# Kernel tuning notes

Hardware: AMD Instinct MI355X
Metric: run time of the kernel (lower is better)

## Reference

```python
import jax, jax.numpy as jnp
import numpy as np

B, T, D, H = 8, 2048, 1024, 128  # batch, seq (== block_size), n_embd, head_size


def setup_inputs() -> dict:
    key = jax.random.key(0)
    kx, kq, kk, kv = jax.random.split(key, 4)
    s = D ** -0.5  # rough linear-init scale
    return {
        "x": jax.random.normal(kx, (B, T, D), dtype=jnp.float32),
        "Wq": jax.random.normal(kq, (D, H), dtype=jnp.float32) * s,
        "Wk": jax.random.normal(kk, (D, H), dtype=jnp.float32) * s,
        "Wv": jax.random.normal(kv, (D, H), dtype=jnp.float32) * s,
    }


def reference(x, Wq, Wk, Wv):
    # Linear projections (no bias)
    q = x @ Wq  # [B, T, H]
    k = x @ Wk  # [B, T, H]
    v = x @ Wv  # [B, T, H]
    scale = k.shape[-1] ** -0.5
    scores = jnp.einsum("bth,bsh->bts", q, k) * scale  # [B, T, T]
    # causal mask from tril buffer
    causal = jnp.tril(jnp.ones((T, T), dtype=bool))
    scores = jnp.where(causal, scores, jnp.finfo(scores.dtype).min)
    att = jax.nn.softmax(scores, axis=-1)
    out = jnp.einsum("bts,bsh->bth", att, v)  # [B, T, H]
    return out
```

## Files before the change

### kernel.cpp

```cpp
#include <hip/hip_runtime.h>
#include <hip/hip_bf16.h>
#include <stdint.h>

typedef float f32x4 __attribute__((ext_vector_type(4)));
typedef __bf16 bf16x8 __attribute__((ext_vector_type(8)));

#define T_SEQ 2048
#define D_EMB 1024
#define H_DIM 128
#define NBATCH 8
#define NTOK 16384

typedef __attribute__((address_space(3))) uint32_t lds_u32;
typedef const __attribute__((address_space(1))) uint32_t glb_u32;

#define DPPF(x, ctrl)                                                    \
  __int_as_float(__builtin_amdgcn_update_dpp(                            \
      0, __float_as_int(x), (ctrl), 0xF, 0xF, true))


__global__ __launch_bounds__(256) void prep_w_kernel(
    const float* __restrict__ Wq, const float* __restrict__ Wk,
    const float* __restrict__ Wv, __hip_bfloat16* __restrict__ Wt) {
  const int mat = blockIdx.x >> 7;
  const int h = blockIdx.x & 127;
  const float* W = (mat == 0) ? Wq : ((mat == 1) ? Wk : Wv);
  __hip_bfloat16* dst = Wt + (size_t)(mat * 128 + h) * D_EMB;
  for (int k = threadIdx.x; k < D_EMB; k += 256)
    dst[k] = __float2bfloat16(W[(size_t)k * H_DIM + h]);
}

__global__ __launch_bounds__(512) void proj_kernel(
    const float* __restrict__ x, const __hip_bfloat16* __restrict__ Wt,
    __hip_bfloat16* __restrict__ qb, __hip_bfloat16* __restrict__ kb,
    __hip_bfloat16* __restrict__ vt) {
  __shared__ __align__(16) __hip_bfloat16 As[64 * 64];
  __shared__ __align__(16) __hip_bfloat16 Bs[384 * 64];
  const int tid = threadIdx.x;
  const int wave = tid >> 6;
  const int lane = tid & 63;
  const int g = lane >> 4;
  const int lr = lane & 15;
  const int m0 = blockIdx.x * 64;
  const int wc = wave * 48;

  f32x4 acc[4][3];
#pragma unroll
  for (int m = 0; m < 4; ++m)
#pragma unroll
    for (int n = 0; n < 3; ++n) acc[m][n] = f32x4{0.f, 0.f, 0.f, 0.f};

  const int arow = tid >> 3;
  const int acol = (tid & 7) * 8;
  const float* asrc = x + (size_t)(m0 + arow) * D_EMB + acol;
  __hip_bfloat16* adst = &As[arow * 64 + (acol ^ ((arow & 7) * 8))];

  for (int k0 = 0; k0 < D_EMB; k0 += 64) {
    __syncthreads();
#pragma unroll
    for (int i = 0; i < 6; ++i) {
      const int e = (i * 512 + tid) * 8;
      const int br = e >> 6;
      const int bc = e & 63;
      __builtin_amdgcn_global_load_lds(
          (glb_u32*)(uintptr_t)(Wt + (size_t)br * D_EMB + k0 + bc),
          (lds_u32*)(uintptr_t)(&Bs[e]), 16, 0, 0);
    }
    {
      const float4 f0 = *reinterpret_cast<const float4*>(asrc + k0);
      const float4 f1 = *reinterpret_cast<const float4*>(asrc + k0 + 4);
      union { bf16x8 v; __hip_bfloat16 h[8]; } u;
      u.h[0] = __float2bfloat16(f0.x);
      u.h[1] = __float2bfloat16(f0.y);
      u.h[2] = __float2bfloat16(f0.z);
      u.h[3] = __float2bfloat16(f0.w);
      u.h[4] = __float2bfloat16(f1.x);
      u.h[5] = __float2bfloat16(f1.y);
      u.h[6] = __float2bfloat16(f1.z);
      u.h[7] = __float2bfloat16(f1.w);
      *reinterpret_cast<bf16x8*>(adst) = u.v;
    }
    __syncthreads();
#pragma unroll
    for (int kk = 0; kk < 2; ++kk) {
      bf16x8 a[4];
#pragma unroll
      for (int m = 0; m < 4; ++m) {
        const int row = m * 16 + lr;
        a[m] = *reinterpret_cast<const bf16x8*>(
            &As[row * 64 + ((kk * 32 + g * 8) ^ ((row & 7) * 8))]);
      }
#pragma unroll
      for (int n = 0; n < 3; ++n) {
        bf16x8 b = *reinterpret_cast<const bf16x8*>(
            &Bs[(size_t)(wc + n * 16 + lr) * 64 + kk * 32 + g * 8]);
#pragma unroll
        for (int m = 0; m < 4; ++m)
          acc[m][n] =
              __builtin_amdgcn_mfma_f32_16x16x32_bf16(a[m], b, acc[m][n], 0, 0, 0);
      }
    }
  }

#pragma unroll
  for (int n = 0; n < 3; ++n) {
    const int ng = wc + n * 16 + lr;
    const int head = ng >> 7;
    const int h = ng & 127;
#pragma unroll
    for (int m = 0; m < 4; ++m) {
#pragma unroll
      for (int r = 0; r < 4; ++r) {
        const int row = m0 + m * 16 + g * 4 + r;
        const __hip_bfloat16 val = __float2bfloat16(acc[m][n][r]);
        if (head == 0) {
          qb[(size_t)row * H_DIM + h] = val;
        } else if (head == 1) {
          kb[(size_t)row * H_DIM + h] = val;
        } else {
          const int bi = row >> 11;
          const int t = row & (T_SEQ - 1);
          vt[((size_t)bi * H_DIM + h) * T_SEQ + t] = val;
        }
      }
    }
  }
}

__global__ __launch_bounds__(512) void attn_kernel(
    const __hip_bfloat16* __restrict__ qb, const __hip_bfloat16* __restrict__ kb,
    const __hip_bfloat16* __restrict__ vt, float* __restrict__ out,
    float* __restrict__ PA_O, float* __restrict__ PA_ml,
    float* __restrict__ PB_O, float* __restrict__ PB_ml) {
  __shared__ __align__(16) __hip_bfloat16 KV[2][16384];
  __shared__ __align__(16) __hip_bfloat16 Pl[8][16][40];
  __shared__ float Obuf[4][16][132];
  __shared__ float mbuf[8][16];
  __shared__ float lbuf[8][16];

  const int tid = threadIdx.x;
  const int wave = tid >> 6;
  const int lane = tid & 63;
  const int g = lane >> 4;
  const int lr = lane & 15;
  const int qt = wave >> 1;
  const int kp = wave & 1;
  const int idx = blockIdx.x;
  const int b = idx & 7;
  const int u = idx >> 3;

  const __hip_bfloat16* qB = qb + (size_t)b * T_SEQ * H_DIM;
  const __hip_bfloat16* kB = kb + (size_t)b * T_SEQ * H_DIM;
  const __hip_bfloat16* vB = vt + (size_t)b * H_DIM * T_SEQ;
  const float scale = 0.08838834764831845f;

  auto stage = [&](__hip_bfloat16* buf, int s0) {
#pragma unroll
    for (int i = 0; i < 2; ++i) {
      const int uu = tid + i * 512;
      const int row = uu >> 4, grp = uu & 15;
      __builtin_amdgcn_global_load_lds(
          (glb_u32*)(uintptr_t)(kB + (size_t)(s0 + row) * H_DIM +
                                ((grp ^ (row & 15)) * 8)),
          (lds_u32*)(uintptr_t)(buf + uu * 8), 16, 0, 0);
    }
#pragma unroll
    for (int i = 0; i < 2; ++i) {
      const int uu = tid + i * 512;
      const int h = uu >> 3, grp = uu & 7;
      __builtin_amdgcn_global_load_lds(
          (glb_u32*)(uintptr_t)(vB + (size_t)h * T_SEQ + s0 +
                                ((grp ^ (h & 7)) * 8)),
          (lds_u32*)(uintptr_t)(buf + 8192 + uu * 8), 16, 0, 0);
    }
  };

  auto process = [&](int tile, int rr0, int rr1, int mode) {
    const int qrow0 = tile * 64 + qt * 16;
    bf16x8 qf[4];
#pragma unroll
    for (int kt = 0; kt < 4; ++kt)
      qf[kt] = *reinterpret_cast<const bf16x8*>(
          qB + (size_t)(qrow0 + lr) * H_DIM + kt * 32 + g * 8);

    f32x4 oacc[8];
#pragma unroll
    for (int i = 0; i < 8; ++i) oacc[i] = f32x4{0.f, 0.f, 0.f, 0.f};
    float mrow[4] = {-1e30f, -1e30f, -1e30f, -1e30f};
    float lrow[4] = {0.f, 0.f, 0.f, 0.f};

    __hip_bfloat16* bufA = &KV[0][0];
    __hip_bfloat16* bufB = &KV[1][0];
    stage(bufA, rr0 * 64);
    __syncthreads();

    for (int r = rr0; r <= rr1; ++r) {
      if (r < rr1) stage(bufB, (r + 1) * 64);
      const int s0 = r * 64;
      const bool active = (s0 + kp * 32) <= (qrow0 + 15);
      if (active) {
        f32x4 sacc[2];
        sacc[0] = f32x4{0.f, 0.f, 0.f, 0.f};
        sacc[1] = f32x4{0.f, 0.f, 0.f, 0.f};
#pragma unroll
        for (int nt = 0; nt < 2; ++nt) {
          const int kl = kp * 32 + nt * 16 + lr;
          const __hip_bfloat16* kr = bufA + kl * 128;
#pragma unroll
          for (int kt = 0; kt < 4; ++kt) {
            bf16x8 kf = *reinterpret_cast<const bf16x8*>(
                kr + (((kt * 4 + g) ^ (kl & 15)) * 8));
            sacc[nt] = __builtin_amdgcn_mfma_f32_16x16x32_bf16(qf[kt], kf,
                                                               sacc[nt], 0, 0, 0);
          }
        }
        bf16x8 vf[8];
#pragma unroll
        for (int ht = 0; ht < 8; ++ht) {
          const int h = ht * 16 + lr;
          vf[ht] = *reinterpret_cast<const bf16x8*>(
              bufA + 8192 + h * 64 + (((kp * 4 + g) ^ (h & 7)) * 8));
        }
        float sv[2][4];
#pragma unroll
        for (int nt = 0; nt < 2; ++nt)
#pragma unroll
          for (int rr = 0; rr < 4; ++rr) {
            const int key = s0 + kp * 32 + nt * 16 + lr;
            const int qr = qrow0 + g * 4 + rr;
            const float s = sacc[nt][rr] * scale;
            sv[nt][rr] = (key > qr) ? -1e30f : s;
          }
        float pm[4];
#pragma unroll
        for (int rr = 0; rr < 4; ++rr) pm[rr] = fmaxf(sv[0][rr], sv[1][rr]);
#pragma unroll
        for (int rr = 0; rr < 4; ++rr) {
          pm[rr] = fmaxf(pm[rr], DPPF(pm[rr], 0xB1));
          pm[rr] = fmaxf(pm[rr], DPPF(pm[rr], 0x4E));
          pm[rr] = fmaxf(pm[rr], DPPF(pm[rr], 0x141));
          pm[rr] = fmaxf(pm[rr], DPPF(pm[rr], 0x140));
        }
        bool ok = true;
#pragma unroll
        for (int rr = 0; rr < 4; ++rr) ok = ok && (pm[rr] <= mrow[rr] + 8.f);
        if (!__all((int)ok)) {
#pragma unroll
          for (int rr = 0; rr < 4; ++rr) {
            const float mnew = fmaxf(mrow[rr], pm[rr]);
            const float corr = __expf(mrow[rr] - mnew);
            mrow[rr] = mnew;
            lrow[rr] *= corr;
#pragma unroll
            for (int ht = 0; ht < 8; ++ht) oacc[ht][rr] *= corr;
          }
        }
        float rs[4];
#pragma unroll
        for (int rr = 0; rr < 4; ++rr) {
          const float p0 = __expf(sv[0][rr] - mrow[rr]);
          const float p1 = __expf(sv[1][rr] - mrow[rr]);
          Pl[wave][g * 4 + rr][lr] = __float2bfloat16(p0);
          Pl[wave][g * 4 + rr][16 + lr] = __float2bfloat16(p1);
          rs[rr] = p0 + p1;
        }
#pragma unroll
        for (int rr = 0; rr < 4; ++rr) {
          rs[rr] += DPPF(rs[rr], 0xB1);
          rs[rr] += DPPF(rs[rr], 0x4E);
          rs[rr] += DPPF(rs[rr], 0x141);
          rs[rr] += DPPF(rs[rr], 0x140);
        }
#pragma unroll
        for (int rr = 0; rr < 4; ++rr) lrow[rr] += rs[rr];
        bf16x8 pf = *reinterpret_cast<const bf16x8*>(&Pl[wave][lr][g * 8]);
#pragma unroll
        for (int ht = 0; ht < 8; ++ht)
          oacc[ht] = __builtin_amdgcn_mfma_f32_16x16x32_bf16(pf, vf[ht],
                                                             oacc[ht], 0, 0, 0);
      }
      __syncthreads();
      __hip_bfloat16* t = bufA; bufA = bufB; bufB = t;
    }

    if (kp == 1) {
#pragma unroll
      for (int ht = 0; ht < 8; ++ht)
#pragma unroll
        for (int rr = 0; rr < 4; ++rr)
          Obuf[qt][g * 4 + rr][ht * 16 + lr] = oacc[ht][rr];
      if (lr == 0) {
#pragma unroll
        for (int rr = 0; rr < 4; ++rr) {
          mbuf[wave][g * 4 + rr] = mrow[rr];
          lbuf[wave][g * 4 + rr] = lrow[rr];
        }
      }
    }
    __syncthreads();
    if (kp == 0) {
#pragma unroll
      for (int rr = 0; rr < 4; ++rr) {
        const float mB = mbuf[wave + 1][g * 4 + rr];
        const float lB = lbuf[wave + 1][g * 4 + rr];
        const float M = fmaxf(mrow[rr], mB);
        const float a = __expf(mrow[rr] - M);
        const float bt = __expf(mB - M);
        lrow[rr] = a * lrow[rr] + bt * lB;
        mrow[rr] = M;
#pragma unroll
        for (int ht = 0; ht < 8; ++ht)
          oacc[ht][rr] =
              a * oacc[ht][rr] + bt * Obuf[qt][g * 4 + rr][ht * 16 + lr];
      }
      if (mode == 0) {
#pragma unroll
        for (int ht = 0; ht < 8; ++ht)
#pragma unroll
          for (int rr = 0; rr < 4; ++rr) {
            const int qr = qrow0 + g * 4 + rr;
            out[((size_t)b * T_SEQ + qr) * H_DIM + ht * 16 + lr] =
                oacc[ht][rr] / lrow[rr];
          }
      } else {
        float* PO = (mode == 1) ? PA_O : PB_O;
        float* Pm = (mode == 1) ? PA_ml : PB_ml;
        const int slot = tile - 16;
#pragma unroll
        for (int rr = 0; rr < 4; ++rr) {
          const size_t pr = (size_t)(b * 16 + slot) * 64 + qt * 16 + g * 4 + rr;
#pragma unroll
          for (int ht = 0; ht < 8; ++ht)
            PO[pr * 128 + ht * 16 + lr] = oacc[ht][rr];
          if (lr == 0) {
            Pm[pr * 2 + 0] = mrow[rr];
            Pm[pr * 2 + 1] = lrow[rr];
          }
        }
      }
    }
    __syncthreads();
  };

  if (u < 16) {
    process(u, 0, u, 0);
    process(31 - u, 0, 15 - u, 1);
  } else {
    const int v = u - 16;
    process(31 - v, 16 - v, 31 - v, 2);
  }
}

__global__ __launch_bounds__(256) void combine_kernel(
    const float* __restrict__ PA_O, const float* __restrict__ PA_ml,
    const float* __restrict__ PB_O, const float* __restrict__ PB_ml,
    float* __restrict__ out) {
  const int b = blockIdx.x >> 4;
  const int s = blockIdx.x & 15;
  const int tid = threadIdx.x;
  const int row = tid >> 2;
  const int c0 = (tid & 3) * 32;
  const size_t pr = (size_t)(b * 16 + s) * 64 + row;
  const float mA = PA_ml[pr * 2], lA = PA_ml[pr * 2 + 1];
  const float mB = PB_ml[pr * 2], lB = PB_ml[pr * 2 + 1];
  const float M = fmaxf(mA, mB);
  const float a = __expf(mA - M), bb = __expf(mB - M);
  const float inv = 1.f / (a * lA + bb * lB);
  const float* oa = PA_O + pr * 128 + c0;
  const float* ob = PB_O + pr * 128 + c0;
  float* op = out + ((size_t)b * T_SEQ + (16 + s) * 64 + row) * H_DIM + c0;
#pragma unroll
  for (int i = 0; i < 32; i += 4) {
    const float4 x = *reinterpret_cast<const float4*>(oa + i);
    const float4 y = *reinterpret_cast<const float4*>(ob + i);
    float4 z;
    z.x = (a * x.x + bb * y.x) * inv;
    z.y = (a * x.y + bb * y.y) * inv;
    z.z = (a * x.z + bb * y.z) * inv;
    z.w = (a * x.w + bb * y.w) * inv;
    *reinterpret_cast<float4*>(op + i) = z;
  }
}

extern "C" void kernel_launch(void* const* d_in, const int* in_sizes, int n_in,
                              void* d_out, int out_size, void* d_ws, size_t ws_size,
                              hipStream_t stream) {
  const float* x = (const float*)d_in[0];
  const float* Wq = (const float*)d_in[1];
  const float* Wk = (const float*)d_in[2];
  const float* Wv = (const float*)d_in[3];
  float* out = (float*)d_out;

  __hip_bfloat16* Wt = (__hip_bfloat16*)d_ws;
  __hip_bfloat16* qbuf = Wt + (size_t)3 * 128 * 1024;
  __hip_bfloat16* kbuf = qbuf + (size_t)NTOK * H_DIM;
  __hip_bfloat16* vbuf = kbuf + (size_t)NTOK * H_DIM;
  float* fbase = (float*)(vbuf + (size_t)NBATCH * H_DIM * T_SEQ);
  float* PA_O = fbase;
  float* PA_ml = PA_O + (size_t)1048576;
  float* PB_O = PA_ml + 16384;
  float* PB_ml = PB_O + (size_t)1048576;

  hipLaunchKernelGGL(prep_w_kernel, dim3(384), dim3(256), 0, stream, Wq, Wk, Wv, Wt);
  hipLaunchKernelGGL(proj_kernel, dim3(256), dim3(512), 0, stream, x, Wt, qbuf,
                     kbuf, vbuf);
  hipLaunchKernelGGL(attn_kernel, dim3(256), dim3(512), 0, stream, qbuf, kbuf,
                     vbuf, out, PA_O, PA_ml, PB_O, PB_ml);
  hipLaunchKernelGGL(combine_kernel, dim3(128), dim3(256), 0, stream, PA_O,
                     PA_ml, PB_O, PB_ml, out);
}
```

Baseline: 80.53 us.

## Double-buffer projection GEMM tiles and swizzle B tile in LDS

The projection kernel now keeps two LDS buffers for the A and B tiles. It issues the next K-step's global loads (the direct-to-LDS B copy and the x float loads into registers) before running the MFMAs on the current buffer, which leaves one barrier per iteration instead of two. The B tile also gets an XOR swizzle on its 16-byte chunks, applied on the global-address side, to cut LDS bank conflicts on the MFMA operand reads. This doubles LDS use to roughly 112KB per block and adds register pressure from holding the prefetched x values.

```diff
diff --git a/kernel.cpp b/kernel.cpp
--- a/kernel.cpp
+++ b/kernel.cpp
@@ -34,8 +34,8 @@
     const float* __restrict__ x, const __hip_bfloat16* __restrict__ Wt,
     __hip_bfloat16* __restrict__ qb, __hip_bfloat16* __restrict__ kb,
     __hip_bfloat16* __restrict__ vt) {
-  __shared__ __align__(16) __hip_bfloat16 As[64 * 64];
-  __shared__ __align__(16) __hip_bfloat16 Bs[384 * 64];
+  __shared__ __align__(16) __hip_bfloat16 As[2][64 * 64];
+  __shared__ __align__(16) __hip_bfloat16 Bs[2][384 * 64];
   const int tid = threadIdx.x;
   const int wave = tid >> 6;
   const int lane = tid & 63;
@@ -53,34 +53,33 @@
   const int arow = tid >> 3;
   const int acol = (tid & 7) * 8;
   const float* asrc = x + (size_t)(m0 + arow) * D_EMB + acol;
-  __hip_bfloat16* adst = &As[arow * 64 + (acol ^ ((arow & 7) * 8))];
-
-  for (int k0 = 0; k0 < D_EMB; k0 += 64) {
-    __syncthreads();
+
+  auto stageB = [&](int buf, int k0) {
 #pragma unroll
     for (int i = 0; i < 6; ++i) {
-      const int e = (i * 512 + tid) * 8;
-      const int br = e >> 6;
-      const int bc = e & 63;
+      const int u = i * 512 + tid;
+      const int row = u >> 3;
+      const int chunk = u & 7;
       __builtin_amdgcn_global_load_lds(
-          (glb_u32*)(uintptr_t)(Wt + (size_t)br * D_EMB + k0 + bc),
-          (lds_u32*)(uintptr_t)(&Bs[e]), 16, 0, 0);
-    }
-    {
-      const float4 f0 = *reinterpret_cast<const float4*>(asrc + k0);
-      const float4 f1 = *reinterpret_cast<const float4*>(asrc + k0 + 4);
-      union { bf16x8 v; __hip_bfloat16 h[8]; } u;
-      u.h[0] = __float2bfloat16(f0.x);
-      u.h[1] = __float2bfloat16(f0.y);
-      u.h[2] = __float2bfloat16(f0.z);
-      u.h[3] = __float2bfloat16(f0.w);
-      u.h[4] = __float2bfloat16(f1.x);
-      u.h[5] = __float2bfloat16(f1.y);
-      u.h[6] = __float2bfloat16(f1.z);
-      u.h[7] = __float2bfloat16(f1.w);
-      *reinterpret_cast<bf16x8*>(adst) = u.v;
-    }
-    __syncthreads();
+          (glb_u32*)(uintptr_t)(Wt + (size_t)row * D_EMB + k0 +
+                                ((chunk ^ (row & 7)) * 8)),
+          (lds_u32*)(uintptr_t)(&Bs[buf][row * 64 + chunk * 8]), 16, 0, 0);
+    }
+  };
+  auto writeA = [&](int buf, float4 f0, float4 f1) {
+    union { bf16x8 v; __hip_bfloat16 h[8]; } u;
+    u.h[0] = __float2bfloat16(f0.x);
+    u.h[1] = __float2bfloat16(f0.y);
+    u.h[2] = __float2bfloat16(f0.z);
+    u.h[3] = __float2bfloat16(f0.w);
+    u.h[4] = __float2bfloat16(f1.x);
+    u.h[5] = __float2bfloat16(f1.y);
+    u.h[6] = __float2bfloat16(f1.z);
+    u.h[7] = __float2bfloat16(f1.w);
+    *reinterpret_cast<bf16x8*>(
+        &As[buf][arow * 64 + (acol ^ ((arow & 7) * 8))]) = u.v;
+  };
+  auto compute = [&](int buf) {
 #pragma unroll
     for (int kk = 0; kk < 2; ++kk) {
       bf16x8 a[4];
@@ -88,18 +87,42 @@
       for (int m = 0; m < 4; ++m) {
         const int row = m * 16 + lr;
         a[m] = *reinterpret_cast<const bf16x8*>(
-            &As[row * 64 + ((kk * 32 + g * 8) ^ ((row & 7) * 8))]);
+            &As[buf][row * 64 + ((kk * 32 + g * 8) ^ ((row & 7) * 8))]);
       }
 #pragma unroll
       for (int n = 0; n < 3; ++n) {
+        const int row = wc + n * 16 + lr;
         bf16x8 b = *reinterpret_cast<const bf16x8*>(
-            &Bs[(size_t)(wc + n * 16 + lr) * 64 + kk * 32 + g * 8]);
+            &Bs[buf][row * 64 + (((kk * 4 + g) ^ (row & 7)) * 8)]);
 #pragma unroll
         for (int m = 0; m < 4; ++m)
           acc[m][n] =
               __builtin_amdgcn_mfma_f32_16x16x32_bf16(a[m], b, acc[m][n], 0, 0, 0);
       }
     }
+  };
+
+  {
+    float4 f0 = *reinterpret_cast<const float4*>(asrc);
+    float4 f1 = *reinterpret_cast<const float4*>(asrc + 4);
+    stageB(0, 0);
+    writeA(0, f0, f1);
+  }
+  __syncthreads();
+
+  int cur = 0;
+  for (int k = 0; k < 16; ++k) {
+    float4 f0, f1;
+    if (k < 15) {
+      const int k0n = (k + 1) * 64;
+      f0 = *reinterpret_cast<const float4*>(asrc + k0n);
+      f1 = *reinterpret_cast<const float4*>(asrc + k0n + 4);
+      stageB(cur ^ 1, k0n);
+    }
+    compute(cur);
+    if (k < 15) writeA(cur ^ 1, f0, f1);
+    __syncthreads();
+    cur ^= 1;
   }
 
 #pragma unroll
```

Measured after the change: 71.62 us. 1.12x faster.
